# Kernel optimization log

Measured on AMD Instinct MI355X. Metric: run time of the kernel, lower is better.

The kernel has to match this reference:

```python
import jax, jax.numpy as jnp
import numpy as np

N = 100000
E = 1600000
F_IN = 50
VALUE = 10
HID = 4 * VALUE  # 40
C = 121


def _gat_conv(x, edge_index, W, att_src, att_dst, bias, heads, out_dim, concat):
    """PyG GATConv: add self-loops, LeakyReLU(0.2) scores, softmax over incoming
    edges per destination node, attention-weighted scatter-add aggregation."""
    n = x.shape[0]
    src = jnp.concatenate([edge_index[0], jnp.arange(n)])  # self loops
    dst = jnp.concatenate([edge_index[1], jnp.arange(n)])
    xw = (x @ W).reshape(n, heads, out_dim)            # [N,H,D]
    a_src = (xw * att_src).sum(-1)                     # [N,H]
    a_dst = (xw * att_dst).sum(-1)                     # [N,H]
    e = jax.nn.leaky_relu(a_src[src] + a_dst[dst], 0.2)  # [E+N,H]
    # segment softmax over destination nodes (numerically stable)
    emax = jax.ops.segment_max(e, dst, num_segments=n)
    ex = jnp.exp(e - emax[dst])
    denom = jax.ops.segment_sum(ex, dst, num_segments=n)
    alpha = ex / denom[dst]                            # [E+N,H]
    msg = xw[src] * alpha[..., None]                   # [E+N,H,D]
    agg = jax.ops.segment_sum(msg, dst, num_segments=n)  # [N,H,D]
    if concat:
        agg = agg.reshape(n, heads * out_dim)
    else:
        agg = agg.mean(axis=1)
    return agg + bias


def setup_inputs() -> dict:
    key = jax.random.key(0)
    ks = jax.random.split(key, 20)
    s = 0.1
    inp = {
        "x": jax.random.normal(ks[0], (N, F_IN), jnp.float32),
        "edge_index": jax.random.randint(ks[1], (2, E), 0, N, jnp.int64)
        if jax.config.jax_enable_x64 else jax.random.randint(ks[1], (2, E), 0, N, jnp.int32),
        # conv1: GATConv(50 -> 10, heads=4, concat)
        "W1": jax.random.normal(ks[2], (F_IN, 4 * VALUE), jnp.float32) * s,
        "as1": jax.random.normal(ks[3], (4, VALUE), jnp.float32) * s,
        "ad1": jax.random.normal(ks[4], (4, VALUE), jnp.float32) * s,
        "b1": jnp.zeros((4 * VALUE,), jnp.float32),
        "lw1": jax.random.normal(ks[5], (F_IN, HID), jnp.float32) * s,
        "lb1": jnp.zeros((HID,), jnp.float32),
        # conv2: GATConv(40 -> 10, heads=4, concat)
        "W2": jax.random.normal(ks[6], (HID, 4 * VALUE), jnp.float32) * s,
        "as2": jax.random.normal(ks[7], (4, VALUE), jnp.float32) * s,
        "ad2": jax.random.normal(ks[8], (4, VALUE), jnp.float32) * s,
        "b2": jnp.zeros((4 * VALUE,), jnp.float32),
        "lw2": jax.random.normal(ks[9], (HID, HID), jnp.float32) * s,
        "lb2": jnp.zeros((HID,), jnp.float32),
        # conv3: GATConv(40 -> 121, heads=6, concat=False -> mean)
        "W3": jax.random.normal(ks[10], (HID, 6 * C), jnp.float32) * s,
        "as3": jax.random.normal(ks[11], (6, C), jnp.float32) * s,
        "ad3": jax.random.normal(ks[12], (6, C), jnp.float32) * s,
        "b3": jnp.zeros((C,), jnp.float32),
        "lw3": jax.random.normal(ks[13], (HID, C), jnp.float32) * s,
        "lb3": jnp.zeros((C,), jnp.float32),
    }
    return inp


def reference(x, edge_index, W1, as1, ad1, b1, lw1, lb1,
              W2, as2, ad2, b2, lw2, lb2,
              W3, as3, ad3, b3, lw3, lb3):
    h = jax.nn.elu(_gat_conv(x, edge_index, W1, as1, ad1, b1, 4, VALUE, True)
                   + x @ lw1 + lb1)
    h = jax.nn.elu(_gat_conv(h, edge_index, W2, as2, ad2, b2, 4, VALUE, True)
                   + h @ lw2 + lb2)
    out = _gat_conv(h, edge_index, W3, as3, ad3, b3, 6, C, False) + h @ lw3 + lb3
    return out
```

## Files before the change

### kernel.cpp

```cpp
#include <hip/hip_runtime.h>
#include <hip/hip_bf16.h>
#include <math.h>


#define NN 100000
#define NE 1600000
#define NT (NE + NN)
#define FIN 50
#define HID 40
#define COUT 121

#define NB 128
#define NPB 782
#define EPB 8192

typedef __attribute__((ext_vector_type(8))) short bf16x8;
typedef __attribute__((ext_vector_type(4))) float f32x4;

__device__ __forceinline__ float lrelu(float x) { return fmaxf(x, 0.2f * x); }
__device__ __forceinline__ float elu1(float x)  { return x > 0.f ? x : __expf(x) - 1.f; }

__global__ __launch_bounds__(256)
void zero_bcnt_kernel(int* __restrict__ bcnt) {
    int t = threadIdx.x;
    if (t < NB) bcnt[t] = 0;
}

__global__ __launch_bounds__(256)
void bin_count_kernel(const int* __restrict__ edst, int* __restrict__ bcnt) {
    __shared__ int h[NB];
    int t = threadIdx.x;
    if (t < NB) h[t] = 0;
    __syncthreads();
    int e0 = blockIdx.x * EPB;
    for (int q = 0; q < EPB; q += 256) {
        int e = e0 + q + t;
        if (e < NE) atomicAdd(&h[edst[e] / NPB], 1);
    }
    __syncthreads();
    if (t < NB && h[t]) atomicAdd(&bcnt[t], h[t]);
}

__global__ __launch_bounds__(256)
void bin_scan_kernel(const int* __restrict__ bcnt, int* __restrict__ boff,
                     int* __restrict__ bcur) {
    __shared__ int s[NB];
    int t = threadIdx.x;
    if (t < NB) s[t] = bcnt[t];
    __syncthreads();
    if (t == 0) {
        int run = 0;
        for (int i = 0; i < NB; i++) { int c = s[i]; s[i] = run; run += c; }
        boff[NB] = run;
    }
    __syncthreads();
    if (t < NB) { boff[t] = s[t]; bcur[t] = s[t]; }
}

__global__ __launch_bounds__(256)
void bin_place_kernel(const int* __restrict__ esrc, const int* __restrict__ edst,
                      int* __restrict__ bcur, int* __restrict__ ebuf) {
    __shared__ int h[NB], base[NB], lcur[NB];
    int t = threadIdx.x;
    if (t < NB) h[t] = 0;
    __syncthreads();
    int e0 = blockIdx.x * EPB;
    for (int q = 0; q < EPB; q += 256) {
        int e = e0 + q + t;
        if (e < NE) atomicAdd(&h[edst[e] / NPB], 1);
    }
    __syncthreads();
    if (t < NB) {
        int c = h[t];
        base[t] = c ? atomicAdd(&bcur[t], c) : 0;
        lcur[t] = 0;
    }
    __syncthreads();
    for (int q = 0; q < EPB; q += 256) {
        int e = e0 + q + t;
        if (e < NE) {
            int d = edst[e], s = esrc[e];
            int b = d / NPB;
            int r = atomicAdd(&lcur[b], 1);
            ebuf[base[b] + r] = s | ((d - b * NPB) << 17);
        }
    }
}

__global__ __launch_bounds__(256)
void bucket_deg_kernel(const int* __restrict__ boff, const int* __restrict__ ebuf,
                       int* __restrict__ deg) {
    __shared__ int h[NPB];
    int b = blockIdx.x, t = threadIdx.x;
    for (int i = t; i < NPB; i += 256) h[i] = 0;
    __syncthreads();
    int jb = boff[b], je = boff[b + 1];
    for (int j = jb + t; j < je; j += 256) atomicAdd(&h[ebuf[j] >> 17], 1);
    __syncthreads();
    int n0 = b * NPB;
    for (int i = t; i < NPB; i += 256) {
        int n = n0 + i;
        if (n < NN) deg[n] = h[i] + 1;
    }
}

__global__ __launch_bounds__(256)
void bucket_scatter_kernel(const int* __restrict__ boff, const int* __restrict__ ebuf,
                           const int* __restrict__ off, int* __restrict__ sorted_src) {
    __shared__ int lcur[NPB];
    int b = blockIdx.x, t = threadIdx.x;
    int n0 = b * NPB;
    for (int i = t; i < NPB; i += 256) {
        int n = n0 + i;
        lcur[i] = (n < NN) ? off[n] + 1 : 0;
    }
    __syncthreads();
    int jb = boff[b], je = boff[b + 1];
    for (int j = jb + t; j < je; j += 256) {
        int rec = ebuf[j];
        int p = atomicAdd(&lcur[rec >> 17], 1);
        sorted_src[p] = rec & 0x1FFFF;
    }
}

__global__ __launch_bounds__(256)
void scan_block_kernel(const int* __restrict__ deg, int* __restrict__ off,
                       int* __restrict__ bsum) {
    __shared__ int s[256];
    int t = threadIdx.x, b = blockIdx.x, i = b * 256 + t;
    int v = (i < NN) ? deg[i] : 0;
    s[t] = v; __syncthreads();
#pragma unroll
    for (int o = 1; o < 256; o <<= 1) {
        int x = (t >= o) ? s[t - o] : 0;
        __syncthreads();
        s[t] += x;
        __syncthreads();
    }
    if (i < NN) off[i] = s[t] - v;
    if (t == 255) bsum[b] = s[255];
}

__global__ __launch_bounds__(256)
void scan_bsum_kernel(const int* __restrict__ bsum, int* __restrict__ bscan, int nb) {
    __shared__ int s[256];
    int t = threadIdx.x;
    int carry = 0;
    int nc = (nb + 255) / 256;
    for (int c = 0; c < nc; c++) {
        int i = c * 256 + t;
        int v = (i < nb) ? bsum[i] : 0;
        s[t] = v; __syncthreads();
#pragma unroll
        for (int o = 1; o < 256; o <<= 1) {
            int x = (t >= o) ? s[t - o] : 0;
            __syncthreads();
            s[t] += x;
            __syncthreads();
        }
        if (i < nb) bscan[i] = carry + s[t] - v;
        carry += s[255];
        __syncthreads();
    }
}

__global__ __launch_bounds__(256)
void place_kernel(int* __restrict__ off, const int* __restrict__ bscan,
                  int* __restrict__ sorted_src) {
    int i = blockIdx.x * 256 + threadIdx.x;
    if (i == 0) off[NN] = NT;
    if (i < NN) {
        int o = off[i] + bscan[i >> 8];
        off[i] = o;
        sorted_src[o] = i;
    }
}

__global__ __launch_bounds__(256)
void fold_B12_kernel(const float* __restrict__ W, const float* __restrict__ lw,
                     const float* __restrict__ as_, const float* __restrict__ ad_,
                     float* __restrict__ B, int F) {
    int t = blockIdx.x * 256 + threadIdx.x;
    if (t >= F * 88) return;
    int f = t / 88, j = t - f * 88;
    float v = 0.f;
    if (j < 40) v = W[f * 40 + j];
    else if (j < 80) v = lw[f * 40 + (j - 40)];
    else if (j < 84) {
        int h = j - 80; float s = 0.f;
        for (int d = 0; d < 10; d++) s += W[f * 40 + h * 10 + d] * as_[h * 10 + d];
        v = s;
    } else {
        int h = j - 84; float s = 0.f;
        for (int d = 0; d < 10; d++) s += W[f * 40 + h * 10 + d] * ad_[h * 10 + d];
        v = s;
    }
    B[t] = v;
}

__global__ __launch_bounds__(256)
void fold_B3_kernel(const float* __restrict__ W3, const float* __restrict__ as3,
                    const float* __restrict__ ad3, float* __restrict__ B) {
    int t = blockIdx.x * 256 + threadIdx.x;
    if (t >= 40 * 12) return;
    int f = t / 12, k = t - f * 12;
    float s = 0.f;
    if (k < 6) {
        int h = k;
        for (int c = 0; c < COUT; c++) s += W3[f * 726 + h * COUT + c] * as3[h * COUT + c];
    } else {
        int h = k - 6;
        for (int c = 0; c < COUT; c++) s += W3[f * 726 + h * COUT + c] * ad3[h * COUT + c];
    }
    B[t] = s;
}

__global__ __launch_bounds__(256)
void fold_Bf_kernel(const float* __restrict__ W3, const float* __restrict__ lw3,
                    __hip_bfloat16* __restrict__ Bf) {
    int t = blockIdx.x * 256 + threadIdx.x;
    if (t >= 9 * 8 * 64 * 8) return;
    int j = t & 7, lane = (t >> 3) & 63, ct = (t >> 9) & 7, kt = t >> 12;
    int k = kt * 32 + (lane >> 4) * 8 + j;
    int c = ct * 16 + (lane & 15);
    float v = 0.f;
    if (c < COUT) {
        if (k < 240) {
            int h = k / 40, f = k - h * 40;
            v = W3[f * 726 + h * COUT + c];
        } else if (k < 280) {
            int f = k - 240;
            v = lw3[f * COUT + c];
        }
    }
    Bf[t] = __float2bfloat16(v);
}

template <int F>
__global__ __launch_bounds__(256)
void feature12_kernel(const float* __restrict__ A, const float* __restrict__ B,
                      const float* __restrict__ bias, const float* __restrict__ lbias,
                      float* __restrict__ xw, float* __restrict__ agg,
                      float* __restrict__ asrc, float* __restrict__ adst) {
    __shared__ float sB[F * 88];
    const int t = threadIdx.x;
    for (int i = t; i < F * 88; i += 256) sB[i] = B[i];

    const int lane = t & 63;
    const int p = __builtin_amdgcn_readfirstlane(t >> 6);
    const int r = blockIdx.x * 64 + lane;
    const bool valid = r < NN;
    const int rr = valid ? r : NN - 1;

    float a[F];
    if (F % 4 == 0) {
        const float4* A4 = reinterpret_cast<const float4*>(A + (size_t)rr * F);
#pragma unroll
        for (int q = 0; q < F / 4; q++) {
            float4 v = A4[q];
            a[4 * q] = v.x; a[4 * q + 1] = v.y; a[4 * q + 2] = v.z; a[4 * q + 3] = v.w;
        }
    } else {
        const float2* A2 = reinterpret_cast<const float2*>(A + (size_t)rr * F);
#pragma unroll
        for (int q = 0; q < F / 2; q++) {
            float2 v = A2[q];
            a[2 * q] = v.x; a[2 * q + 1] = v.y;
        }
        if (F & 1) a[F - 1] = A[(size_t)rr * F + F - 1];
    }
    __syncthreads();

    for (int g = p; g < 11; g += 4) {
        const int j0 = g * 8;
        float acc[8];
#pragma unroll
        for (int k = 0; k < 8; k++) acc[k] = 0.f;
#pragma unroll
        for (int f = 0; f < F; f++) {
            float av = a[f];
            float4 b0 = *reinterpret_cast<const float4*>(&sB[f * 88 + j0]);
            float4 b1 = *reinterpret_cast<const float4*>(&sB[f * 88 + j0 + 4]);
            acc[0] += av * b0.x; acc[1] += av * b0.y;
            acc[2] += av * b0.z; acc[3] += av * b0.w;
            acc[4] += av * b1.x; acc[5] += av * b1.y;
            acc[6] += av * b1.z; acc[7] += av * b1.w;
        }
        if (!valid) continue;
        if (j0 < 40) {
            *reinterpret_cast<float4*>(xw + (size_t)r * 40 + j0) =
                make_float4(acc[0], acc[1], acc[2], acc[3]);
            *reinterpret_cast<float4*>(xw + (size_t)r * 40 + j0 + 4) =
                make_float4(acc[4], acc[5], acc[6], acc[7]);
        } else if (j0 < 80) {
            int j = j0 - 40;
#pragma unroll
            for (int k = 0; k < 8; k++) acc[k] += bias[j + k] + lbias[j + k];
            *reinterpret_cast<float4*>(agg + (size_t)r * 40 + j) =
                make_float4(acc[0], acc[1], acc[2], acc[3]);
            *reinterpret_cast<float4*>(agg + (size_t)r * 40 + j + 4) =
                make_float4(acc[4], acc[5], acc[6], acc[7]);
        } else {
            *reinterpret_cast<float4*>(asrc + (size_t)r * 8) =
                make_float4(acc[0], acc[1], acc[2], acc[3]);
            *reinterpret_cast<float4*>(adst + (size_t)r * 8) =
                make_float4(acc[4], acc[5], acc[6], acc[7]);
        }
    }
}

__global__ __launch_bounds__(256)
void feature3_kernel(const float* __restrict__ A, const float* __restrict__ B,
                     float* __restrict__ asrc, float* __restrict__ adst,
                     __hip_bfloat16* __restrict__ zb, __hip_bfloat16* __restrict__ hp) {
    int r = blockIdx.x * 256 + threadIdx.x;
    if (r >= NN) return;
    float a[40];
    const float4* A4 = reinterpret_cast<const float4*>(A + (size_t)r * 40);
#pragma unroll
    for (int q = 0; q < 10; q++) {
        float4 v = A4[q];
        a[4 * q] = v.x; a[4 * q + 1] = v.y; a[4 * q + 2] = v.z; a[4 * q + 3] = v.w;
    }
    __hip_bfloat16* zr = zb + (size_t)r * 288 + 240;
    __hip_bfloat16* hr = hp + (size_t)r * 40;
#pragma unroll
    for (int f = 0; f < 40; f++) {
        __hip_bfloat16 v = __float2bfloat16(a[f]);
        zr[f] = v;
        hr[f] = v;
    }
#pragma unroll
    for (int f = 40; f < 48; f++) zr[f] = __float2bfloat16(0.f);

    float acc[12];
#pragma unroll
    for (int k = 0; k < 12; k++) acc[k] = 0.f;
#pragma unroll
    for (int f = 0; f < 40; f++) {
        float av = a[f];
#pragma unroll
        for (int k = 0; k < 12; k++) acc[k] += av * B[f * 12 + k];
    }
    *reinterpret_cast<float4*>(asrc + (size_t)r * 8) = make_float4(acc[0], acc[1], acc[2], acc[3]);
    *reinterpret_cast<float2*>(asrc + (size_t)r * 8 + 4) = make_float2(acc[4], acc[5]);
    *reinterpret_cast<float4*>(adst + (size_t)r * 8) = make_float4(acc[6], acc[7], acc[8], acc[9]);
    *reinterpret_cast<float2*>(adst + (size_t)r * 8 + 4) = make_float2(acc[10], acc[11]);
}

__global__ __launch_bounds__(256)
void ew4_kernel(const int* __restrict__ off, const int* __restrict__ srt,
                const float* __restrict__ asrc, const float* __restrict__ adst,
                float* __restrict__ w4) {
    int wid = ((blockIdx.x * 256 + threadIdx.x) >> 6);
    int d = __builtin_amdgcn_readfirstlane(wid);
    if (d >= NN) return;
    int lane = threadIdx.x & 63;
    float4 b = *reinterpret_cast<const float4*>(adst + (size_t)d * 8);
    int jb = off[d], je = off[d + 1];
    for (int j = jb + lane; j < je; j += 64) {
        int s = srt[j];
        float4 a = *reinterpret_cast<const float4*>(asrc + (size_t)s * 8);
        float4 w;
        w.x = __expf(lrelu(a.x + b.x));
        w.y = __expf(lrelu(a.y + b.y));
        w.z = __expf(lrelu(a.z + b.z));
        w.w = __expf(lrelu(a.w + b.w));
        *reinterpret_cast<float4*>(w4 + (size_t)j * 4) = w;
    }
}

__global__ __launch_bounds__(256)
void ew6_kernel(const int* __restrict__ off, const int* __restrict__ srt,
                const float* __restrict__ asrc, const float* __restrict__ adst,
                float* __restrict__ w6) {
    int wid = ((blockIdx.x * 256 + threadIdx.x) >> 6);
    int d = __builtin_amdgcn_readfirstlane(wid);
    if (d >= NN) return;
    int lane = threadIdx.x & 63;
    float4 b0 = *reinterpret_cast<const float4*>(adst + (size_t)d * 8);
    float2 b1 = *reinterpret_cast<const float2*>(adst + (size_t)d * 8 + 4);
    int jb = off[d], je = off[d + 1];
    for (int j = jb + lane; j < je; j += 64) {
        int s = srt[j];
        float4 a0 = *reinterpret_cast<const float4*>(asrc + (size_t)s * 8);
        float2 a1 = *reinterpret_cast<const float2*>(asrc + (size_t)s * 8 + 4);
        float w0 = __expf(lrelu(a0.x + b0.x));
        float w1 = __expf(lrelu(a0.y + b0.y));
        float w2 = __expf(lrelu(a0.z + b0.z));
        float w3 = __expf(lrelu(a0.w + b0.w));
        float w4_ = __expf(lrelu(a1.x + b1.x));
        float w5 = __expf(lrelu(a1.y + b1.y));
        float* wp = w6 + (size_t)j * 6;
        *reinterpret_cast<float4*>(wp)     = make_float4(w0, w1, w2, w3);
        *reinterpret_cast<float2*>(wp + 4) = make_float2(w4_, w5);
    }
}

__global__ __launch_bounds__(256)
void agg4_csr_kernel(const int* __restrict__ off, const int* __restrict__ srt,
                     const float* __restrict__ w4,
                     const float* __restrict__ xw, float* agg) {
    int wid = ((blockIdx.x * 256 + threadIdx.x) >> 6);
    int d = __builtin_amdgcn_readfirstlane(wid);
    if (d >= NN) return;
    int lane = threadIdx.x & 63;
    bool act = lane < 40;
    int f = act ? lane : 0;
    int hh = f / 10;
    int jb = off[d], je = off[d + 1];
    float acc = 0.f, ds = 0.f;
    int j = jb;
    for (; j + 3 < je; j += 4) {
        int s0 = srt[j], s1 = srt[j + 1], s2 = srt[j + 2], s3 = srt[j + 3];
        float w0 = w4[(size_t)(j + 0) * 4 + hh];
        float w1 = w4[(size_t)(j + 1) * 4 + hh];
        float w2 = w4[(size_t)(j + 2) * 4 + hh];
        float w3 = w4[(size_t)(j + 3) * 4 + hh];
        float x0 = xw[(size_t)s0 * 40 + f], x1 = xw[(size_t)s1 * 40 + f];
        float x2 = xw[(size_t)s2 * 40 + f], x3 = xw[(size_t)s3 * 40 + f];
        acc += w0 * x0; acc += w1 * x1; acc += w2 * x2; acc += w3 * x3;
        ds += (w0 + w1) + (w2 + w3);
    }
    for (; j < je; ++j) {
        int s = srt[j];
        float w = w4[(size_t)j * 4 + hh];
        acc += w * xw[(size_t)s * 40 + f];
        ds += w;
    }
    if (act) {
        float v = agg[(size_t)d * 40 + f] + acc / ds;
        agg[(size_t)d * 40 + f] = elu1(v);
    }
}

__global__ __launch_bounds__(256)
void z6_csr_kernel(const int* __restrict__ off, const int* __restrict__ srt,
                   const float* __restrict__ w6,
                   const __hip_bfloat16* __restrict__ hp, __hip_bfloat16* zb) {
    int wid = ((blockIdx.x * 256 + threadIdx.x) >> 6);
    int d = __builtin_amdgcn_readfirstlane(wid);
    if (d >= NN) return;
    int lane = threadIdx.x & 63;
    bool act = lane < 40;
    int f = act ? lane : 0;
    int jb = off[d], je = off[d + 1];
    float acc[6], ds[6];
#pragma unroll
    for (int h = 0; h < 6; h++) { acc[h] = 0.f; ds[h] = 0.f; }
    int j = jb;
    for (; j + 1 < je; j += 2) {
        int s0 = srt[j], s1 = srt[j + 1];
        float hv0 = __bfloat162float(hp[(size_t)s0 * 40 + f]);
        float hv1 = __bfloat162float(hp[(size_t)s1 * 40 + f]);
        const float* wp = w6 + (size_t)j * 6;
#pragma unroll
        for (int h = 0; h < 6; h++) {
            float w0 = wp[h], w1 = wp[6 + h];
            acc[h] += w0 * hv0; acc[h] += w1 * hv1;
            ds[h] += w0 + w1;
        }
    }
    for (; j < je; ++j) {
        int s = srt[j];
        float hv = __bfloat162float(hp[(size_t)s * 40 + f]);
        const float* wp = w6 + (size_t)j * 6;
#pragma unroll
        for (int h = 0; h < 6; h++) {
            acc[h] += wp[h] * hv;
            ds[h] += wp[h];
        }
    }
    if (act) {
#pragma unroll
        for (int h = 0; h < 6; h++)
            zb[(size_t)d * 288 + h * 40 + f] =
                __float2bfloat16(acc[h] / ds[h] * (1.0f / 6.0f));
    }
}

__global__ __launch_bounds__(256)
void zgemm_mfma_kernel(const __hip_bfloat16* __restrict__ Ab,
                       const __hip_bfloat16* __restrict__ Bf,
                       const float* __restrict__ b3, const float* __restrict__ lb3,
                       float* __restrict__ out) {
    const int t = threadIdx.x;
    const int lane = t & 63, w = t >> 6;
    const int wr = w & 1, wc = w >> 1;
    const int n0 = blockIdx.x * 128;
    const short* As = (const short*)Ab;
    const short* Bs = (const short*)Bf;

    f32x4 acc[4][4];
#pragma unroll
    for (int i = 0; i < 4; i++)
#pragma unroll
        for (int j = 0; j < 4; j++) acc[i][j] = (f32x4){0.f, 0.f, 0.f, 0.f};

    const int arow = n0 + wr * 64 + (lane & 15);
    const int koff = (lane >> 4) * 8;

    for (int kk = 0; kk < 9; kk++) {
        bf16x8 af[4], bfr[4];
#pragma unroll
        for (int i = 0; i < 4; i++) {
            int r = arow + i * 16; if (r > NN - 1) r = NN - 1;
            af[i] = *(const bf16x8*)(As + (size_t)r * 288 + kk * 32 + koff);
        }
#pragma unroll
        for (int j = 0; j < 4; j++) {
            int ct = wc * 4 + j;
            bfr[j] = *(const bf16x8*)(Bs + (((size_t)kk * 8 + ct) * 64 + lane) * 8);
        }
#pragma unroll
        for (int i = 0; i < 4; i++)
#pragma unroll
            for (int j = 0; j < 4; j++)
                acc[i][j] = __builtin_amdgcn_mfma_f32_16x16x32_bf16(af[i], bfr[j], acc[i][j], 0, 0, 0);
    }

    const int c_base = wc * 64 + (lane & 15);
    const int r_quad = (lane >> 4) * 4;
#pragma unroll
    for (int j = 0; j < 4; j++) {
        int c = c_base + j * 16;
        if (c >= COUT) continue;
        float bias = b3[c] + lb3[c];
#pragma unroll
        for (int i = 0; i < 4; i++) {
            int nb = n0 + wr * 64 + i * 16 + r_quad;
#pragma unroll
            for (int q = 0; q < 4; q++) {
                int n = nb + q;
                if (n < NN) out[(size_t)n * COUT + c] = acc[i][j][q] + bias;
            }
        }
    }
}

extern "C" void kernel_launch(void* const* d_in, const int* in_sizes, int n_in,
                              void* d_out, int out_size, void* d_ws, size_t ws_size,
                              hipStream_t stream) {
    const float* x   = (const float*)d_in[0];
    const int*   ei  = (const int*)d_in[1];
    const float* W1  = (const float*)d_in[2];
    const float* as1 = (const float*)d_in[3];
    const float* ad1 = (const float*)d_in[4];
    const float* b1  = (const float*)d_in[5];
    const float* lw1 = (const float*)d_in[6];
    const float* lb1 = (const float*)d_in[7];
    const float* W2  = (const float*)d_in[8];
    const float* as2 = (const float*)d_in[9];
    const float* ad2 = (const float*)d_in[10];
    const float* b2  = (const float*)d_in[11];
    const float* lw2 = (const float*)d_in[12];
    const float* lb2 = (const float*)d_in[13];
    const float* W3  = (const float*)d_in[14];
    const float* as3 = (const float*)d_in[15];
    const float* ad3 = (const float*)d_in[16];
    const float* b3  = (const float*)d_in[17];
    const float* lw3 = (const float*)d_in[18];
    const float* lb3 = (const float*)d_in[19];
    float* out = (float*)d_out;
    float* ws  = (float*)d_ws;

    const int* esrc = ei;
    const int* edst = ei + NE;

    float* xw   = ws;
    float* agg  = ws + 4000000;
    float* asrc = ws + 8000000;
    float* adst = ws + 8800000;
    float* Bc   = ws + 9600000;
    __hip_bfloat16* Bf = (__hip_bfloat16*)(ws + 9608000);
    __hip_bfloat16* zb = (__hip_bfloat16*)(ws + 9628000);
    float* w4 = ws + 9628000;
    __hip_bfloat16* hp = (__hip_bfloat16*)ws;
    int* ib     = (int*)(ws + 24028000);
    int* deg    = ib;
    int* off    = ib + 100352;
    int* bcnt   = ib + 200704;
    int* boff   = ib + 200832;
    int* bcur   = ib + 200992;
    int* bsum   = ib + 300704;
    int* bscan  = ib + 301216;
    int* sorted = ib + 301728;
    int* ebuf   = ib + 2001728;
    float* w6   = ws + 27729728;

    const int nodeBlocks = (NN + 255) / 256;
    const int binBlocks  = (NE + EPB - 1) / EPB;
    const int waveBlocks = NN / 4;
    const int featBlocks = (NN + 63) / 64;

    zero_bcnt_kernel<<<1, 256, 0, stream>>>(bcnt);
    bin_count_kernel<<<binBlocks, 256, 0, stream>>>(edst, bcnt);
    bin_scan_kernel<<<1, 256, 0, stream>>>(bcnt, boff, bcur);
    bin_place_kernel<<<binBlocks, 256, 0, stream>>>(esrc, edst, bcur, ebuf);
    bucket_deg_kernel<<<NB, 256, 0, stream>>>(boff, ebuf, deg);
    scan_block_kernel<<<nodeBlocks, 256, 0, stream>>>(deg, off, bsum);
    scan_bsum_kernel<<<1, 256, 0, stream>>>(bsum, bscan, nodeBlocks);
    place_kernel<<<nodeBlocks, 256, 0, stream>>>(off, bscan, sorted);
    bucket_scatter_kernel<<<NB, 256, 0, stream>>>(boff, ebuf, off, sorted);

    fold_B12_kernel<<<(FIN * 88 + 255) / 256, 256, 0, stream>>>(W1, lw1, as1, ad1, Bc, FIN);
    feature12_kernel<FIN><<<featBlocks, 256, 0, stream>>>(x, Bc, b1, lb1, xw, agg, asrc, adst);
    ew4_kernel<<<waveBlocks, 256, 0, stream>>>(off, sorted, asrc, adst, w4);
    agg4_csr_kernel<<<waveBlocks, 256, 0, stream>>>(off, sorted, w4, xw, agg);

    fold_B12_kernel<<<(HID * 88 + 255) / 256, 256, 0, stream>>>(W2, lw2, as2, ad2, Bc, HID);
    feature12_kernel<HID><<<featBlocks, 256, 0, stream>>>(agg, Bc, b2, lb2, xw, agg, asrc, adst);
    ew4_kernel<<<waveBlocks, 256, 0, stream>>>(off, sorted, asrc, adst, w4);
    agg4_csr_kernel<<<waveBlocks, 256, 0, stream>>>(off, sorted, w4, xw, agg);

    fold_B3_kernel<<<(40 * 12 + 255) / 256, 256, 0, stream>>>(W3, as3, ad3, Bc);
    fold_Bf_kernel<<<(9 * 8 * 64 * 8 + 255) / 256, 256, 0, stream>>>(W3, lw3, Bf);
    feature3_kernel<<<nodeBlocks, 256, 0, stream>>>(agg, Bc, asrc, adst, zb, hp);
    ew6_kernel<<<waveBlocks, 256, 0, stream>>>(off, sorted, asrc, adst, w6);
    z6_csr_kernel<<<waveBlocks, 256, 0, stream>>>(off, sorted, w6, hp, zb);
    zgemm_mfma_kernel<<<(NN + 127) / 128, 256, 0, stream>>>(zb, Bf, b3, lb3, out);
}
```

Baseline: 606.7 us.

## Fuse edge-weight computation into CSR aggregation kernels via LDS staging

Drops the separate ew4/ew6 kernels that wrote per-edge exp attention weights to global memory. Each wave now loads up to 64 incoming edges per chunk, computes their exp(leaky_relu) weights, and stages them with the source indices in shared memory. The aggregation loop then reads them from LDS. This removes three launches and the global write and read of the per-edge weight arrays, at the cost of some LDS traffic and chunked loops. It relies on wave-synchronous LDS access with no barrier between the staging writes and the reads.

```diff
diff --git a/kernel.cpp b/kernel.cpp
--- a/kernel.cpp
+++ b/kernel.cpp
@@ -349,84 +349,55 @@
 }
 
 __global__ __launch_bounds__(256)
-void ew4_kernel(const int* __restrict__ off, const int* __restrict__ srt,
-                const float* __restrict__ asrc, const float* __restrict__ adst,
-                float* __restrict__ w4) {
-    int wid = ((blockIdx.x * 256 + threadIdx.x) >> 6);
+void agg4_csr_kernel(const int* __restrict__ off, const int* __restrict__ srt,
+                     const float* __restrict__ asrc, const float* __restrict__ adst,
+                     const float* __restrict__ xw, float* agg) {
+    __shared__ float sW[4][64 * 4];
+    __shared__ int   sS[4][64];
+    int t = threadIdx.x;
+    int wslot = t >> 6;
+    int wid = (blockIdx.x * 256 + t) >> 6;
     int d = __builtin_amdgcn_readfirstlane(wid);
     if (d >= NN) return;
-    int lane = threadIdx.x & 63;
-    float4 b = *reinterpret_cast<const float4*>(adst + (size_t)d * 8);
-    int jb = off[d], je = off[d + 1];
-    for (int j = jb + lane; j < je; j += 64) {
-        int s = srt[j];
-        float4 a = *reinterpret_cast<const float4*>(asrc + (size_t)s * 8);
-        float4 w;
-        w.x = __expf(lrelu(a.x + b.x));
-        w.y = __expf(lrelu(a.y + b.y));
-        w.z = __expf(lrelu(a.z + b.z));
-        w.w = __expf(lrelu(a.w + b.w));
-        *reinterpret_cast<float4*>(w4 + (size_t)j * 4) = w;
-    }
-}
-
-__global__ __launch_bounds__(256)
-void ew6_kernel(const int* __restrict__ off, const int* __restrict__ srt,
-                const float* __restrict__ asrc, const float* __restrict__ adst,
-                float* __restrict__ w6) {
-    int wid = ((blockIdx.x * 256 + threadIdx.x) >> 6);
-    int d = __builtin_amdgcn_readfirstlane(wid);
-    if (d >= NN) return;
-    int lane = threadIdx.x & 63;
-    float4 b0 = *reinterpret_cast<const float4*>(adst + (size_t)d * 8);
-    float2 b1 = *reinterpret_cast<const float2*>(adst + (size_t)d * 8 + 4);
-    int jb = off[d], je = off[d + 1];
-    for (int j = jb + lane; j < je; j += 64) {
-        int s = srt[j];
-        float4 a0 = *reinterpret_cast<const float4*>(asrc + (size_t)s * 8);
-        float2 a1 = *reinterpret_cast<const float2*>(asrc + (size_t)s * 8 + 4);
-        float w0 = __expf(lrelu(a0.x + b0.x));
-        float w1 = __expf(lrelu(a0.y + b0.y));
-        float w2 = __expf(lrelu(a0.z + b0.z));
-        float w3 = __expf(lrelu(a0.w + b0.w));
-        float w4_ = __expf(lrelu(a1.x + b1.x));
-        float w5 = __expf(lrelu(a1.y + b1.y));
-        float* wp = w6 + (size_t)j * 6;
-        *reinterpret_cast<float4*>(wp)     = make_float4(w0, w1, w2, w3);
-        *reinterpret_cast<float2*>(wp + 4) = make_float2(w4_, w5);
-    }
-}
-
-__global__ __launch_bounds__(256)
-void agg4_csr_kernel(const int* __restrict__ off, const int* __restrict__ srt,
-                     const float* __restrict__ w4,
-                     const float* __restrict__ xw, float* agg) {
-    int wid = ((blockIdx.x * 256 + threadIdx.x) >> 6);
-    int d = __builtin_amdgcn_readfirstlane(wid);
-    if (d >= NN) return;
-    int lane = threadIdx.x & 63;
+    int lane = t & 63;
     bool act = lane < 40;
     int f = act ? lane : 0;
     int hh = f / 10;
+    float4 bv = *reinterpret_cast<const float4*>(adst + (size_t)d * 8);
     int jb = off[d], je = off[d + 1];
     float acc = 0.f, ds = 0.f;
-    int j = jb;
-    for (; j + 3 < je; j += 4) {
-        int s0 = srt[j], s1 = srt[j + 1], s2 = srt[j + 2], s3 = srt[j + 3];
-        float w0 = w4[(size_t)(j + 0) * 4 + hh];
-        float w1 = w4[(size_t)(j + 1) * 4 + hh];
-        float w2 = w4[(size_t)(j + 2) * 4 + hh];
-        float w3 = w4[(size_t)(j + 3) * 4 + hh];
-        float x0 = xw[(size_t)s0 * 40 + f], x1 = xw[(size_t)s1 * 40 + f];
-        float x2 = xw[(size_t)s2 * 40 + f], x3 = xw[(size_t)s3 * 40 + f];
-        acc += w0 * x0; acc += w1 * x1; acc += w2 * x2; acc += w3 * x3;
-        ds += (w0 + w1) + (w2 + w3);
-    }
-    for (; j < je; ++j) {
-        int s = srt[j];
-        float w = w4[(size_t)j * 4 + hh];
-        acc += w * xw[(size_t)s * 40 + f];
-        ds += w;
+    for (int c0 = jb; c0 < je; c0 += 64) {
+        int cnt = je - c0; if (cnt > 64) cnt = 64;
+        if (lane < cnt) {
+            int s = srt[c0 + lane];
+            sS[wslot][lane] = s;
+            float4 a = *reinterpret_cast<const float4*>(asrc + (size_t)s * 8);
+            float4 w;
+            w.x = __expf(lrelu(a.x + bv.x));
+            w.y = __expf(lrelu(a.y + bv.y));
+            w.z = __expf(lrelu(a.z + bv.z));
+            w.w = __expf(lrelu(a.w + bv.w));
+            *reinterpret_cast<float4*>(&sW[wslot][lane * 4]) = w;
+        }
+        int j = 0;
+        for (; j + 3 < cnt; j += 4) {
+            int s0 = sS[wslot][j], s1 = sS[wslot][j + 1];
+            int s2 = sS[wslot][j + 2], s3 = sS[wslot][j + 3];
+            float w0 = sW[wslot][(j + 0) * 4 + hh];
+            float w1 = sW[wslot][(j + 1) * 4 + hh];
+            float w2 = sW[wslot][(j + 2) * 4 + hh];
+            float w3 = sW[wslot][(j + 3) * 4 + hh];
+            float x0 = xw[(size_t)s0 * 40 + f], x1 = xw[(size_t)s1 * 40 + f];
+            float x2 = xw[(size_t)s2 * 40 + f], x3 = xw[(size_t)s3 * 40 + f];
+            acc += w0 * x0; acc += w1 * x1; acc += w2 * x2; acc += w3 * x3;
+            ds += (w0 + w1) + (w2 + w3);
+        }
+        for (; j < cnt; ++j) {
+            int s = sS[wslot][j];
+            float w = sW[wslot][j * 4 + hh];
+            acc += w * xw[(size_t)s * 40 + f];
+            ds += w;
+        }
     }
     if (act) {
         float v = agg[(size_t)d * 40 + f] + acc / ds;
@@ -436,39 +407,60 @@
 
 __global__ __launch_bounds__(256)
 void z6_csr_kernel(const int* __restrict__ off, const int* __restrict__ srt,
-                   const float* __restrict__ w6,
+                   const float* __restrict__ asrc, const float* __restrict__ adst,
                    const __hip_bfloat16* __restrict__ hp, __hip_bfloat16* zb) {
-    int wid = ((blockIdx.x * 256 + threadIdx.x) >> 6);
+    __shared__ float sW[4][64 * 6];
+    __shared__ int   sS[4][64];
+    int t = threadIdx.x;
+    int wslot = t >> 6;
+    int wid = (blockIdx.x * 256 + t) >> 6;
     int d = __builtin_amdgcn_readfirstlane(wid);
     if (d >= NN) return;
-    int lane = threadIdx.x & 63;
+    int lane = t & 63;
     bool act = lane < 40;
     int f = act ? lane : 0;
+    float4 bv0 = *reinterpret_cast<const float4*>(adst + (size_t)d * 8);
+    float2 bv1 = *reinterpret_cast<const float2*>(adst + (size_t)d * 8 + 4);
     int jb = off[d], je = off[d + 1];
     float acc[6], ds[6];
 #pragma unroll
     for (int h = 0; h < 6; h++) { acc[h] = 0.f; ds[h] = 0.f; }
-    int j = jb;
-    for (; j + 1 < je; j += 2) {
-        int s0 = srt[j], s1 = srt[j + 1];
-        float hv0 = __bfloat162float(hp[(size_t)s0 * 40 + f]);
-        float hv1 = __bfloat162float(hp[(size_t)s1 * 40 + f]);
-        const float* wp = w6 + (size_t)j * 6;
-#pragma unroll
-        for (int h = 0; h < 6; h++) {
-            float w0 = wp[h], w1 = wp[6 + h];
-            acc[h] += w0 * hv0; acc[h] += w1 * hv1;
-            ds[h] += w0 + w1;
-        }
-    }
-    for (; j < je; ++j) {
-        int s = srt[j];
-        float hv = __bfloat162float(hp[(size_t)s * 40 + f]);
-        const float* wp = w6 + (size_t)j * 6;
-#pragma unroll
-        for (int h = 0; h < 6; h++) {
-            acc[h] += wp[h] * hv;
-            ds[h] += wp[h];
+    for (int c0 = jb; c0 < je; c0 += 64) {
+        int cnt = je - c0; if (cnt > 64) cnt = 64;
+        if (lane < cnt) {
+            int s = srt[c0 + lane];
+            sS[wslot][lane] = s;
+            float4 a0 = *reinterpret_cast<const float4*>(asrc + (size_t)s * 8);
+            float2 a1 = *reinterpret_cast<const float2*>(asrc + (size_t)s * 8 + 4);
+            float* wp = &sW[wslot][lane * 6];
+            *reinterpret_cast<float4*>(wp) = make_float4(
+                __expf(lrelu(a0.x + bv0.x)), __expf(lrelu(a0.y + bv0.y)),
+                __expf(lrelu(a0.z + bv0.z)), __expf(lrelu(a0.w + bv0.w)));
+            *reinterpret_cast<float2*>(wp + 4) = make_float2(
+                __expf(lrelu(a1.x + bv1.x)), __expf(lrelu(a1.y + bv1.y)));
+        }
+        int j = 0;
+        for (; j + 1 < cnt; j += 2) {
+            int s0 = sS[wslot][j], s1 = sS[wslot][j + 1];
+            float hv0 = __bfloat162float(hp[(size_t)s0 * 40 + f]);
+            float hv1 = __bfloat162float(hp[(size_t)s1 * 40 + f]);
+            const float* wp = &sW[wslot][j * 6];
+#pragma unroll
+            for (int h = 0; h < 6; h++) {
+                float w0 = wp[h], w1 = wp[6 + h];
+                acc[h] += w0 * hv0; acc[h] += w1 * hv1;
+                ds[h] += w0 + w1;
+            }
+        }
+        for (; j < cnt; ++j) {
+            int s = sS[wslot][j];
+            float hv = __bfloat162float(hp[(size_t)s * 40 + f]);
+            const float* wp = &sW[wslot][j * 6];
+#pragma unroll
+            for (int h = 0; h < 6; h++) {
+                acc[h] += wp[h] * hv;
+                ds[h] += wp[h];
+            }
         }
     }
     if (act) {
@@ -574,7 +566,6 @@
     float* Bc   = ws + 9600000;
     __hip_bfloat16* Bf = (__hip_bfloat16*)(ws + 9608000);
     __hip_bfloat16* zb = (__hip_bfloat16*)(ws + 9628000);
-    float* w4 = ws + 9628000;
     __hip_bfloat16* hp = (__hip_bfloat16*)ws;
     int* ib     = (int*)(ws + 24028000);
     int* deg    = ib;
@@ -586,7 +577,6 @@
     int* bscan  = ib + 301216;
     int* sorted = ib + 301728;
     int* ebuf   = ib + 2001728;
-    float* w6   = ws + 27729728;
 
     const int nodeBlocks = (NN + 255) / 256;
     const int binBlocks  = (NE + EPB - 1) / EPB;
@@ -605,18 +595,15 @@
 
     fold_B12_kernel<<<(FIN * 88 + 255) / 256, 256, 0, stream>>>(W1, lw1, as1, ad1, Bc, FIN);
     feature12_kernel<FIN><<<featBlocks, 256, 0, stream>>>(x, Bc, b1, lb1, xw, agg, asrc, adst);
-    ew4_kernel<<<waveBlocks, 256, 0, stream>>>(off, sorted, asrc, adst, w4);
-    agg4_csr_kernel<<<waveBlocks, 256, 0, stream>>>(off, sorted, w4, xw, agg);
+    agg4_csr_kernel<<<waveBlocks, 256, 0, stream>>>(off, sorted, asrc, adst, xw, agg);
 
     fold_B12_kernel<<<(HID * 88 + 255) / 256, 256, 0, stream>>>(W2, lw2, as2, ad2, Bc, HID);
     feature12_kernel<HID><<<featBlocks, 256, 0, stream>>>(agg, Bc, b2, lb2, xw, agg, asrc, adst);
-    ew4_kernel<<<waveBlocks, 256, 0, stream>>>(off, sorted, asrc, adst, w4);
-    agg4_csr_kernel<<<waveBlocks, 256, 0, stream>>>(off, sorted, w4, xw, agg);
+    agg4_csr_kernel<<<waveBlocks, 256, 0, stream>>>(off, sorted, asrc, adst, xw, agg);
 
     fold_B3_kernel<<<(40 * 12 + 255) / 256, 256, 0, stream>>>(W3, as3, ad3, Bc);
     fold_Bf_kernel<<<(9 * 8 * 64 * 8 + 255) / 256, 256, 0, stream>>>(W3, lw3, Bf);
     feature3_kernel<<<nodeBlocks, 256, 0, stream>>>(agg, Bc, asrc, adst, zb, hp);
-    ew6_kernel<<<waveBlocks, 256, 0, stream>>>(off, sorted, asrc, adst, w6);
-    z6_csr_kernel<<<waveBlocks, 256, 0, stream>>>(off, sorted, w6, hp, zb);
+    z6_csr_kernel<<<waveBlocks, 256, 0, stream>>>(off, sorted, asrc, adst, hp, zb);
     zgemm_mfma_kernel<<<(NN + 127) / 128, 256, 0, stream>>>(zb, Bf, b3, lb3, out);
 }
```

Measured after the change: 546.9 us. -9.9%, faster.
